# Performance work log

Hardware: AMD Instinct MI355X
Metric: run time of the kernel (lower is better)

The kernel has to match this reference:

```python
import jax, jax.numpy as jnp
import numpy as np

DIM = 1024
DEPTH = 7
PAR = 8
N_NODES = 2 ** (DEPTH + 1) - 1  # 255
WIDTH = PAR * N_NODES  # 2040


def setup_inputs() -> dict:
    key = jax.random.key(0)
    k1, k2, k3, k4 = jax.random.split(key, 4)
    init_k = float(np.sqrt(1.0 / DIM))
    init_k2 = float(np.sqrt(1.0 / ((DEPTH + 1) * PAR)))
    oldx = jax.random.normal(k1, (4, 2048, DIM), dtype=jnp.float32)
    W_in = jax.random.uniform(k2, (WIDTH, DIM), jnp.float32, -init_k, init_k)
    b_in = jax.random.uniform(k3, (WIDTH,), jnp.float32, -init_k, init_k)
    W_out = jax.random.uniform(k4, (DIM, WIDTH), jnp.float32, -init_k2, init_k2)
    return {"oldx": oldx, "W_in": W_in, "b_in": b_in, "W_out": W_out}


def reference(oldx, W_in, b_in, W_out):
    x = oldx.reshape(-1, DIM)                      # [B, dim]
    B = x.shape[0]
    logits = x @ W_in.T + b_in                     # [B, width] dense GEMM over ALL nodes
    decisions = (logits > 0).astype(jnp.int32).reshape(B, PAR, N_NODES)
    acts = jax.nn.silu(logits).reshape(B, PAR, N_NODES)

    # Tree traversal: mark root, then descend DEPTH levels by each node's sign bit.
    current = jnp.zeros((B, PAR), dtype=jnp.int32)
    dmap = jax.nn.one_hot(current, N_NODES, dtype=acts.dtype)  # root node marked
    for d in range(DEPTH):
        cur_platform = 2 ** d - 1
        next_platform = 2 ** (d + 1) - 1
        moves = jnp.take_along_axis(decisions, current[..., None], axis=2)[..., 0]
        current = (current - cur_platform) * 2 + moves + next_platform
        dmap = dmap + jax.nn.one_hot(current, N_NODES, dtype=acts.dtype)

    masked = acts * jax.lax.stop_gradient(dmap)    # only depth+1 nodes per tree survive
    out = masked.reshape(B, WIDTH) @ W_out.T       # [B, dim]
    return out.reshape(oldx.shape)
```

## Files before the change

### kernel.cpp

```cpp
#include <hip/hip_runtime.h>
#include <math.h>

#define DIM 1024
#define DEPTH 7
#define PAR 8
#define N_NODES 255
#define WIDTH 2040
#define MARGIN 0.03f

#define REPLANE(p) ((((p) & 1) << 3) | ((((p) >> 1) & 1) << 4) | ((((p) >> 2) & 1) << 5))

typedef float  float2v  __attribute__((ext_vector_type(2)));
typedef _Float16 half2v __attribute__((ext_vector_type(2)));

__device__ __forceinline__ unsigned short f32_to_bf16(float f) {
    unsigned int u = __float_as_uint(f);
    u += 0x7fffu + ((u >> 16) & 1u);
    return (unsigned short)(u >> 16);
}
__device__ __forceinline__ float bf_lo(unsigned int u) { return __uint_as_float(u << 16); }
__device__ __forceinline__ float bf_hi(unsigned int u) { return __uint_as_float(u & 0xffff0000u); }

__device__ __forceinline__ half2v as_h2(unsigned int u) {
    union { unsigned int u; half2v h; } c; c.u = u; return c.h;
}
__device__ __forceinline__ unsigned int pack_h2(float a, float b) {
    union { half2v h; unsigned int u; } c;
    c.h = (half2v){(_Float16)a, (_Float16)b};
    return c.u;
}

__device__ __forceinline__ float dot2h(unsigned int a, unsigned int b, float c) {
#if __has_builtin(__builtin_amdgcn_fdot2)
    return __builtin_amdgcn_fdot2(as_h2(a), as_h2(b), c, false);
#else
    half2v ha = as_h2(a), hb = as_h2(b);
    c = fmaf((float)ha.x, (float)hb.x, c);
    return fmaf((float)ha.y, (float)hb.y, c);
#endif
}

__device__ __forceinline__ float foldK(float a, float b, int K) {
    const bool hi = (threadIdx.x & (unsigned)K) != 0;
    const float keep = hi ? b : a;
    const float send = hi ? a : b;
    return keep + __shfl_xor(send, K, 64);
}

__global__ __launch_bounds__(256) void convert_f16_kernel(
    const float* __restrict__ src, unsigned int* __restrict__ dst, int n4)
{
    int i = (int)(blockIdx.x * blockDim.x + threadIdx.x);
    if (i < n4) {
        float4 v = ((const float4*)src)[i];
        uint2 pk;
        pk.x = pack_h2(v.x, v.y);
        pk.y = pack_h2(v.z, v.w);
        ((uint2*)dst)[i] = pk;
    }
}

__global__ __launch_bounds__(256) void transpose_bf16_kernel(
    const float* __restrict__ W_out, unsigned short* __restrict__ WoT)
{
    __shared__ float tile[64][65];
    const int w0 = blockIdx.x * 64;
    const int d0 = blockIdx.y * 64;
    const int tid = (int)threadIdx.x;
    const int sub = tid & 15;
    const int grp = tid >> 4;

    #pragma unroll
    for (int pass = 0; pass < 4; ++pass) {
        const int dl = pass * 16 + grp;
        const int wl = sub * 4;
        const int w = w0 + wl;
        const int d = d0 + dl;
        float4 v = make_float4(0.f, 0.f, 0.f, 0.f);
        if (w + 3 < WIDTH) {
            v = *(const float4*)(W_out + (size_t)d * WIDTH + w);
        } else {
            float t0 = (w + 0 < WIDTH) ? W_out[(size_t)d * WIDTH + w + 0] : 0.f;
            float t1 = (w + 1 < WIDTH) ? W_out[(size_t)d * WIDTH + w + 1] : 0.f;
            float t2 = (w + 2 < WIDTH) ? W_out[(size_t)d * WIDTH + w + 2] : 0.f;
            float t3 = (w + 3 < WIDTH) ? W_out[(size_t)d * WIDTH + w + 3] : 0.f;
            v = make_float4(t0, t1, t2, t3);
        }
        tile[dl][wl + 0] = v.x; tile[dl][wl + 1] = v.y;
        tile[dl][wl + 2] = v.z; tile[dl][wl + 3] = v.w;
    }
    __syncthreads();
    #pragma unroll
    for (int pass = 0; pass < 4; ++pass) {
        const int wl = pass * 16 + grp;
        const int dl = sub * 4;
        const int w = w0 + wl;
        if (w < WIDTH) {
            unsigned int b0 = f32_to_bf16(tile[dl + 0][wl]);
            unsigned int b1 = f32_to_bf16(tile[dl + 1][wl]);
            unsigned int b2 = f32_to_bf16(tile[dl + 2][wl]);
            unsigned int b3 = f32_to_bf16(tile[dl + 3][wl]);
            uint2 pk;
            pk.x = b0 | (b1 << 16);
            pk.y = b2 | (b3 << 16);
            *(uint2*)(WoT + (size_t)w * DIM + d0 + dl) = pk;
        }
    }
}

__global__ __launch_bounds__(256) void fff_f16_kernel(
    const float* __restrict__ x,
    const float* __restrict__ W_in,
    const float* __restrict__ b_in,
    const unsigned int* __restrict__ Wh,
    const unsigned short* __restrict__ WoT,
    float* __restrict__ out,
    int B)
{
    const int wave = (int)((blockIdx.x * blockDim.x + threadIdx.x) >> 6);
    const int lane = (int)(threadIdx.x & 63);
    if (wave >= B) return;

    const float* xr = x + (size_t)wave * DIM;
    unsigned int xp[8];
    {
        float4 a0 = *(const float4*)(xr + lane * 8 + 0);
        float4 a1 = *(const float4*)(xr + lane * 8 + 4);
        float4 a2 = *(const float4*)(xr + 512 + lane * 8 + 0);
        float4 a3 = *(const float4*)(xr + 512 + lane * 8 + 4);
        xp[0] = pack_h2(a0.x, a0.y);
        xp[1] = pack_h2(a0.z, a0.w);
        xp[2] = pack_h2(a1.x, a1.y);
        xp[3] = pack_h2(a1.z, a1.w);
        xp[4] = pack_h2(a2.x, a2.y);
        xp[5] = pack_h2(a2.z, a2.w);
        xp[6] = pack_h2(a3.x, a3.y);
        xp[7] = pack_h2(a3.z, a3.w);
    }

    float2v acc2[8];
    #pragma unroll
    for (int i = 0; i < 8; ++i) acc2[i] = (float2v){0.f, 0.f};

    unsigned long long nodes = 0ULL;
    const int myp = ((lane >> 3) & 1) | (((lane >> 4) & 1) << 1) | (((lane >> 5) & 1) << 2);

    #pragma unroll 1
    for (int d = 0; d <= DEPTH; ++d) {
        int gidx[PAR];
        float partial[PAR];

        #pragma unroll
        for (int p = 0; p < PAR; ++p) {
            const int np = (int)((nodes >> (8 * p)) & 0xffULL);
            gidx[p] = p * N_NODES + np;
            const unsigned int* wr = Wh + (size_t)gidx[p] * (DIM / 2);
            const uint4 u0 = *(const uint4*)(wr + lane * 4);
            const uint4 u1 = *(const uint4*)(wr + 256 + lane * 4);
            float s = 0.f;
            s = dot2h(xp[0], u0.x, s);
            s = dot2h(xp[1], u0.y, s);
            s = dot2h(xp[2], u0.z, s);
            s = dot2h(xp[3], u0.w, s);
            s = dot2h(xp[4], u1.x, s);
            s = dot2h(xp[5], u1.y, s);
            s = dot2h(xp[6], u1.z, s);
            s = dot2h(xp[7], u1.w, s);
            partial[p] = s;
        }

        const float c01 = foldK(partial[0], partial[1], 8);
        const float c23 = foldK(partial[2], partial[3], 8);
        const float c45 = foldK(partial[4], partial[5], 8);
        const float c67 = foldK(partial[6], partial[7], 8);
        const float d0f = foldK(c01, c23, 16);
        const float d1f = foldK(c45, c67, 16);
        float e = foldK(d0f, d1f, 32);
        e += __shfl_xor(e, 1, 64);
        e += __shfl_xor(e, 2, 64);
        e += __shfl_xor(e, 4, 64);

        const int ga = (lane & 8) ? gidx[1] : gidx[0];
        const int gb = (lane & 8) ? gidx[3] : gidx[2];
        const int gc = (lane & 8) ? gidx[5] : gidx[4];
        const int gd = (lane & 8) ? gidx[7] : gidx[6];
        const int ge = (lane & 16) ? gb : ga;
        const int gf = (lane & 16) ? gd : gc;
        const int gmine = (lane & 32) ? gf : ge;
        float my = e + b_in[gmine];

        if (d < DEPTH) {
            const unsigned long long bal = __ballot(fabsf(my) < MARGIN);
            unsigned rm = 0;
            #pragma unroll
            for (int p = 0; p < PAR; ++p)
                rm |= ((unsigned)((bal >> REPLANE(p)) & 1ULL)) << p;
            if (rm) {
                const float4 fa = *(const float4*)(xr + lane * 8 + 0);
                const float4 fb = *(const float4*)(xr + lane * 8 + 4);
                const float4 fc = *(const float4*)(xr + 512 + lane * 8 + 0);
                const float4 fd = *(const float4*)(xr + 512 + lane * 8 + 4);
                while (rm) {
                    const int p = __builtin_ctz(rm); rm &= (rm - 1u);
                    const int np = (int)((nodes >> (8 * p)) & 0xffULL);
                    const int gi = p * N_NODES + np;
                    const float* wr = W_in + (size_t)gi * DIM;
                    const float4 wa = *(const float4*)(wr + lane * 8 + 0);
                    const float4 wb = *(const float4*)(wr + lane * 8 + 4);
                    const float4 wc = *(const float4*)(wr + 512 + lane * 8 + 0);
                    const float4 wd = *(const float4*)(wr + 512 + lane * 8 + 4);
                    float s = 0.f;
                    s = fmaf(fa.x, wa.x, s); s = fmaf(fa.y, wa.y, s);
                    s = fmaf(fa.z, wa.z, s); s = fmaf(fa.w, wa.w, s);
                    s = fmaf(fb.x, wb.x, s); s = fmaf(fb.y, wb.y, s);
                    s = fmaf(fb.z, wb.z, s); s = fmaf(fb.w, wb.w, s);
                    s = fmaf(fc.x, wc.x, s); s = fmaf(fc.y, wc.y, s);
                    s = fmaf(fc.z, wc.z, s); s = fmaf(fc.w, wc.w, s);
                    s = fmaf(fd.x, wd.x, s); s = fmaf(fd.y, wd.y, s);
                    s = fmaf(fd.z, wd.z, s); s = fmaf(fd.w, wd.w, s);
                    #pragma unroll
                    for (int off = 32; off >= 1; off >>= 1)
                        s += __shfl_xor(s, off, 64);
                    const float lf = s + b_in[gi];
                    my = (myp == p) ? lf : my;
                }
            }
        }

        const float act_mine = my / (1.0f + __expf(-my));
        const unsigned long long pos = __ballot(my > 0.0f);

        float act[PAR];
        #pragma unroll
        for (int p = 0; p < PAR; ++p)
            act[p] = __shfl(act_mine, REPLANE(p), 64);

        #pragma unroll
        for (int p = 0; p < PAR; ++p) {
            const unsigned short* wo = WoT + (size_t)gidx[p] * DIM;
            const uint4 u0 = *(const uint4*)(wo + lane * 8);
            const uint4 u1 = *(const uint4*)(wo + 512 + lane * 8);
            const float2v a2 = (float2v){act[p], act[p]};
            acc2[0] += a2 * (float2v){bf_lo(u0.x), bf_hi(u0.x)};
            acc2[1] += a2 * (float2v){bf_lo(u0.y), bf_hi(u0.y)};
            acc2[2] += a2 * (float2v){bf_lo(u0.z), bf_hi(u0.z)};
            acc2[3] += a2 * (float2v){bf_lo(u0.w), bf_hi(u0.w)};
            acc2[4] += a2 * (float2v){bf_lo(u1.x), bf_hi(u1.x)};
            acc2[5] += a2 * (float2v){bf_lo(u1.y), bf_hi(u1.y)};
            acc2[6] += a2 * (float2v){bf_lo(u1.z), bf_hi(u1.z)};
            acc2[7] += a2 * (float2v){bf_lo(u1.w), bf_hi(u1.w)};

            if (d < DEPTH) {
                const int np = (int)((nodes >> (8 * p)) & 0xffULL);
                const unsigned long long nn = (unsigned long long)
                    (2 * np + 1 + (int)((pos >> REPLANE(p)) & 1ULL));
                nodes = (nodes & ~(0xffULL << (8 * p))) | (nn << (8 * p));
            }
        }
    }

    float* orow = out + (size_t)wave * DIM;
    *(float4*)(orow + lane * 8 + 0) =
        make_float4(acc2[0].x, acc2[0].y, acc2[1].x, acc2[1].y);
    *(float4*)(orow + lane * 8 + 4) =
        make_float4(acc2[2].x, acc2[2].y, acc2[3].x, acc2[3].y);
    *(float4*)(orow + 512 + lane * 8 + 0) =
        make_float4(acc2[4].x, acc2[4].y, acc2[5].x, acc2[5].y);
    *(float4*)(orow + 512 + lane * 8 + 4) =
        make_float4(acc2[6].x, acc2[6].y, acc2[7].x, acc2[7].y);
}

__global__ __launch_bounds__(256) void fff_fallback_kernel(
    const float* __restrict__ x, const float* __restrict__ W_in,
    const float* __restrict__ b_in, const float* __restrict__ W_out,
    float* __restrict__ out, int B)
{
    const int wave = (int)((blockIdx.x * blockDim.x + threadIdx.x) >> 6);
    const int lane = (int)(threadIdx.x & 63);
    if (wave >= B) return;

    const float* xr = x + (size_t)wave * DIM;
    float4 x4[4];
    x4[0] = *(const float4*)(xr + lane * 8 + 0);
    x4[1] = *(const float4*)(xr + lane * 8 + 4);
    x4[2] = *(const float4*)(xr + 512 + lane * 8 + 0);
    x4[3] = *(const float4*)(xr + 512 + lane * 8 + 4);

    float acc[16];
    #pragma unroll
    for (int i = 0; i < 16; ++i) acc[i] = 0.f;
    int node[PAR];
    #pragma unroll
    for (int p = 0; p < PAR; ++p) node[p] = 0;

    for (int d = 0; d <= DEPTH; ++d) {
        #pragma unroll
        for (int p = 0; p < PAR; ++p) {
            const int gidx = p * N_NODES + node[p];
            const float* wr = W_in + (size_t)gidx * DIM;
            const float4 wa = *(const float4*)(wr + lane * 8 + 0);
            const float4 wb = *(const float4*)(wr + lane * 8 + 4);
            const float4 wc = *(const float4*)(wr + 512 + lane * 8 + 0);
            const float4 wd = *(const float4*)(wr + 512 + lane * 8 + 4);
            float s = 0.f;
            s = fmaf(x4[0].x, wa.x, s); s = fmaf(x4[0].y, wa.y, s);
            s = fmaf(x4[0].z, wa.z, s); s = fmaf(x4[0].w, wa.w, s);
            s = fmaf(x4[1].x, wb.x, s); s = fmaf(x4[1].y, wb.y, s);
            s = fmaf(x4[1].z, wb.z, s); s = fmaf(x4[1].w, wb.w, s);
            s = fmaf(x4[2].x, wc.x, s); s = fmaf(x4[2].y, wc.y, s);
            s = fmaf(x4[2].z, wc.z, s); s = fmaf(x4[2].w, wc.w, s);
            s = fmaf(x4[3].x, wd.x, s); s = fmaf(x4[3].y, wd.y, s);
            s = fmaf(x4[3].z, wd.z, s); s = fmaf(x4[3].w, wd.w, s);
            #pragma unroll
            for (int off = 32; off >= 1; off >>= 1)
                s += __shfl_xor(s, off, 64);
            const float logit = s + b_in[gidx];
            const float act = logit / (1.0f + __expf(-logit));
            #pragma unroll
            for (int k = 0; k < 2; ++k) {
                #pragma unroll
                for (int j = 0; j < 8; ++j) {
                    const int e = k * 512 + lane * 8 + j;
                    acc[k * 8 + j] = fmaf(act, W_out[(size_t)e * WIDTH + gidx], acc[k * 8 + j]);
                }
            }
            node[p] = 2 * node[p] + 1 + ((logit > 0.0f) ? 1 : 0);
        }
    }

    float* orow = out + (size_t)wave * DIM;
    *(float4*)(orow + lane * 8 + 0)       = make_float4(acc[0],  acc[1],  acc[2],  acc[3]);
    *(float4*)(orow + lane * 8 + 4)       = make_float4(acc[4],  acc[5],  acc[6],  acc[7]);
    *(float4*)(orow + 512 + lane * 8 + 0) = make_float4(acc[8],  acc[9],  acc[10], acc[11]);
    *(float4*)(orow + 512 + lane * 8 + 4) = make_float4(acc[12], acc[13], acc[14], acc[15]);
}

extern "C" void kernel_launch(void* const* d_in, const int* in_sizes, int n_in,
                              void* d_out, int out_size, void* d_ws, size_t ws_size,
                              hipStream_t stream) {
    const float* oldx  = (const float*)d_in[0];
    const float* W_in  = (const float*)d_in[1];
    const float* b_in  = (const float*)d_in[2];
    const float* W_out = (const float*)d_in[3];
    float* out = (float*)d_out;

    const int B = in_sizes[0] / DIM;

    const size_t half = (size_t)WIDTH * DIM * sizeof(unsigned short);
    const bool use_lp = (ws_size >= 2 * half) && (d_ws != nullptr);

    const int blocks = (B + 3) / 4;

    if (use_lp) {
        unsigned short* WoT = (unsigned short*)d_ws;
        unsigned int*   Wh  = (unsigned int*)((char*)d_ws + half);
        dim3 tg((WIDTH + 63) / 64, DIM / 64);
        transpose_bf16_kernel<<<tg, 256, 0, stream>>>(W_out, WoT);
        const int n4 = WIDTH * DIM / 4;
        convert_f16_kernel<<<(n4 + 255) / 256, 256, 0, stream>>>(W_in, Wh, n4);
        fff_f16_kernel<<<blocks, 256, 0, stream>>>(oldx, W_in, b_in, Wh, WoT, out, B);
    } else {
        fff_fallback_kernel<<<blocks, 256, 0, stream>>>(oldx, W_in, b_in, W_out, out, B);
    }
}
```

Before: 185.9 us.

## Fuse weight prep kernels, hoist loads ahead of reductions, store W_out as fp16

The two weight preprocessing kernels (W_out transpose and W_in fp16 conversion) are merged into one launch with a block-range split. In the main kernel, all W_in row loads for a level are issued before the dot products, and half of the W_out row loads are issued before the cross-lane reduction and ballot, to hide memory latency. W_out is now stored in fp16 instead of bf16 with scalar fmaf accumulation, and the near-zero refinement margin is tightened, which reduces fp32 recomputation but risks sign-flip mismatches near zero. The extra live registers for prefetched rows may reduce occupancy.

Result: no change. 182.4 us (-1.9%).

```diff
diff --git a/kernel.cpp b/kernel.cpp
--- a/kernel.cpp
+++ b/kernel.cpp
@@ -6,20 +6,11 @@
 #define PAR 8
 #define N_NODES 255
 #define WIDTH 2040
-#define MARGIN 0.03f
+#define MARGIN 0.01f
 
 #define REPLANE(p) ((((p) & 1) << 3) | ((((p) >> 1) & 1) << 4) | ((((p) >> 2) & 1) << 5))
 
-typedef float  float2v  __attribute__((ext_vector_type(2)));
 typedef _Float16 half2v __attribute__((ext_vector_type(2)));
-
-__device__ __forceinline__ unsigned short f32_to_bf16(float f) {
-    unsigned int u = __float_as_uint(f);
-    u += 0x7fffu + ((u >> 16) & 1u);
-    return (unsigned short)(u >> 16);
-}
-__device__ __forceinline__ float bf_lo(unsigned int u) { return __uint_as_float(u << 16); }
-__device__ __forceinline__ float bf_hi(unsigned int u) { return __uint_as_float(u & 0xffff0000u); }
 
 __device__ __forceinline__ half2v as_h2(unsigned int u) {
     union { unsigned int u; half2v h; } c; c.u = u; return c.h;
@@ -47,63 +38,76 @@
     return keep + __shfl_xor(send, K, 64);
 }
 
-__global__ __launch_bounds__(256) void convert_f16_kernel(
-    const float* __restrict__ src, unsigned int* __restrict__ dst, int n4)
-{
-    int i = (int)(blockIdx.x * blockDim.x + threadIdx.x);
-    if (i < n4) {
-        float4 v = ((const float4*)src)[i];
-        uint2 pk;
-        pk.x = pack_h2(v.x, v.y);
-        pk.y = pack_h2(v.z, v.w);
-        ((uint2*)dst)[i] = pk;
-    }
-}
-
-__global__ __launch_bounds__(256) void transpose_bf16_kernel(
-    const float* __restrict__ W_out, unsigned short* __restrict__ WoT)
+#define PHASE_C_TREE(WLO, WHI, A) do {                                                      \
+    const float a_ = (A); half2v h_;                                                        \
+    h_ = as_h2((WLO).x); acc[0]  = fmaf((float)h_.x, a_, acc[0]);  acc[1]  = fmaf((float)h_.y, a_, acc[1]);  \
+    h_ = as_h2((WLO).y); acc[2]  = fmaf((float)h_.x, a_, acc[2]);  acc[3]  = fmaf((float)h_.y, a_, acc[3]);  \
+    h_ = as_h2((WLO).z); acc[4]  = fmaf((float)h_.x, a_, acc[4]);  acc[5]  = fmaf((float)h_.y, a_, acc[5]);  \
+    h_ = as_h2((WLO).w); acc[6]  = fmaf((float)h_.x, a_, acc[6]);  acc[7]  = fmaf((float)h_.y, a_, acc[7]);  \
+    h_ = as_h2((WHI).x); acc[8]  = fmaf((float)h_.x, a_, acc[8]);  acc[9]  = fmaf((float)h_.y, a_, acc[9]);  \
+    h_ = as_h2((WHI).y); acc[10] = fmaf((float)h_.x, a_, acc[10]); acc[11] = fmaf((float)h_.y, a_, acc[11]); \
+    h_ = as_h2((WHI).z); acc[12] = fmaf((float)h_.x, a_, acc[12]); acc[13] = fmaf((float)h_.y, a_, acc[13]); \
+    h_ = as_h2((WHI).w); acc[14] = fmaf((float)h_.x, a_, acc[14]); acc[15] = fmaf((float)h_.y, a_, acc[15]); \
+} while (0)
+
+#define TRANS_BLOCKS 512
+
+__global__ __launch_bounds__(256) void prep_kernel(
+    const float* __restrict__ W_out,
+    const float* __restrict__ W_in,
+    unsigned short* __restrict__ WoT,
+    unsigned int* __restrict__ Wh)
 {
     __shared__ float tile[64][65];
-    const int w0 = blockIdx.x * 64;
-    const int d0 = blockIdx.y * 64;
-    const int tid = (int)threadIdx.x;
-    const int sub = tid & 15;
-    const int grp = tid >> 4;
-
-    #pragma unroll
-    for (int pass = 0; pass < 4; ++pass) {
-        const int dl = pass * 16 + grp;
-        const int wl = sub * 4;
-        const int w = w0 + wl;
-        const int d = d0 + dl;
-        float4 v = make_float4(0.f, 0.f, 0.f, 0.f);
-        if (w + 3 < WIDTH) {
-            v = *(const float4*)(W_out + (size_t)d * WIDTH + w);
-        } else {
-            float t0 = (w + 0 < WIDTH) ? W_out[(size_t)d * WIDTH + w + 0] : 0.f;
-            float t1 = (w + 1 < WIDTH) ? W_out[(size_t)d * WIDTH + w + 1] : 0.f;
-            float t2 = (w + 2 < WIDTH) ? W_out[(size_t)d * WIDTH + w + 2] : 0.f;
-            float t3 = (w + 3 < WIDTH) ? W_out[(size_t)d * WIDTH + w + 3] : 0.f;
-            v = make_float4(t0, t1, t2, t3);
-        }
-        tile[dl][wl + 0] = v.x; tile[dl][wl + 1] = v.y;
-        tile[dl][wl + 2] = v.z; tile[dl][wl + 3] = v.w;
-    }
-    __syncthreads();
-    #pragma unroll
-    for (int pass = 0; pass < 4; ++pass) {
-        const int wl = pass * 16 + grp;
-        const int dl = sub * 4;
-        const int w = w0 + wl;
-        if (w < WIDTH) {
-            unsigned int b0 = f32_to_bf16(tile[dl + 0][wl]);
-            unsigned int b1 = f32_to_bf16(tile[dl + 1][wl]);
-            unsigned int b2 = f32_to_bf16(tile[dl + 2][wl]);
-            unsigned int b3 = f32_to_bf16(tile[dl + 3][wl]);
+    if (blockIdx.x < TRANS_BLOCKS) {
+        const int w0 = (int)(blockIdx.x & 31) * 64;
+        const int d0 = (int)(blockIdx.x >> 5) * 64;
+        const int tid = (int)threadIdx.x;
+        const int sub = tid & 15;
+        const int grp = tid >> 4;
+
+        #pragma unroll
+        for (int pass = 0; pass < 4; ++pass) {
+            const int dl = pass * 16 + grp;
+            const int wl = sub * 4;
+            const int w = w0 + wl;
+            const int d = d0 + dl;
+            float4 v = make_float4(0.f, 0.f, 0.f, 0.f);
+            if (w + 3 < WIDTH) {
+                v = *(const float4*)(W_out + (size_t)d * WIDTH + w);
+            } else {
+                float t0 = (w + 0 < WIDTH) ? W_out[(size_t)d * WIDTH + w + 0] : 0.f;
+                float t1 = (w + 1 < WIDTH) ? W_out[(size_t)d * WIDTH + w + 1] : 0.f;
+                float t2 = (w + 2 < WIDTH) ? W_out[(size_t)d * WIDTH + w + 2] : 0.f;
+                float t3 = (w + 3 < WIDTH) ? W_out[(size_t)d * WIDTH + w + 3] : 0.f;
+                v = make_float4(t0, t1, t2, t3);
+            }
+            tile[dl][wl + 0] = v.x; tile[dl][wl + 1] = v.y;
+            tile[dl][wl + 2] = v.z; tile[dl][wl + 3] = v.w;
+        }
+        __syncthreads();
+        #pragma unroll
+        for (int pass = 0; pass < 4; ++pass) {
+            const int wl = pass * 16 + grp;
+            const int dl = sub * 4;
+            const int w = w0 + wl;
+            if (w < WIDTH) {
+                uint2 pk;
+                pk.x = pack_h2(tile[dl + 0][wl], tile[dl + 1][wl]);
+                pk.y = pack_h2(tile[dl + 2][wl], tile[dl + 3][wl]);
+                *(uint2*)(WoT + (size_t)w * DIM + d0 + dl) = pk;
+            }
+        }
+    } else {
+        const int n4 = WIDTH * DIM / 4;
+        const int nthr = ((int)gridDim.x - TRANS_BLOCKS) * 256;
+        for (int i = ((int)blockIdx.x - TRANS_BLOCKS) * 256 + (int)threadIdx.x;
+             i < n4; i += nthr) {
+            float4 v = ((const float4*)W_in)[i];
             uint2 pk;
-            pk.x = b0 | (b1 << 16);
-            pk.y = b2 | (b3 << 16);
-            *(uint2*)(WoT + (size_t)w * DIM + d0 + dl) = pk;
+            pk.x = pack_h2(v.x, v.y);
+            pk.y = pack_h2(v.z, v.w);
+            ((uint2*)Wh)[i] = pk;
         }
     }
 }
@@ -138,9 +142,9 @@
         xp[7] = pack_h2(a3.z, a3.w);
     }
 
-    float2v acc2[8];
+    float acc[16];
     #pragma unroll
-    for (int i = 0; i < 8; ++i) acc2[i] = (float2v){0.f, 0.f};
+    for (int i = 0; i < 16; ++i) acc[i] = 0.f;
 
     unsigned long long nodes = 0ULL;
     const int myp = ((lane >> 3) & 1) | (((lane >> 4) & 1) << 1) | (((lane >> 5) & 1) << 2);
@@ -148,25 +152,50 @@
     #pragma unroll 1
     for (int d = 0; d <= DEPTH; ++d) {
         int gidx[PAR];
-        float partial[PAR];
-
         #pragma unroll
         for (int p = 0; p < PAR; ++p) {
             const int np = (int)((nodes >> (8 * p)) & 0xffULL);
             gidx[p] = p * N_NODES + np;
+        }
+
+        const int ga = (lane & 8) ? gidx[1] : gidx[0];
+        const int gb = (lane & 8) ? gidx[3] : gidx[2];
+        const int gc = (lane & 8) ? gidx[5] : gidx[4];
+        const int gd = (lane & 8) ? gidx[7] : gidx[6];
+        const int ge = (lane & 16) ? gb : ga;
+        const int gf = (lane & 16) ? gd : gc;
+        const int gmine = (lane & 32) ? gf : ge;
+        const float bias = b_in[gmine];
+
+        uint4 ua[PAR], ub[PAR];
+        #pragma unroll
+        for (int p = 0; p < PAR; ++p) {
             const unsigned int* wr = Wh + (size_t)gidx[p] * (DIM / 2);
-            const uint4 u0 = *(const uint4*)(wr + lane * 4);
-            const uint4 u1 = *(const uint4*)(wr + 256 + lane * 4);
+            ua[p] = *(const uint4*)(wr + lane * 4);
+            ub[p] = *(const uint4*)(wr + 256 + lane * 4);
+        }
+
+        float partial[PAR];
+        #pragma unroll
+        for (int p = 0; p < PAR; ++p) {
             float s = 0.f;
-            s = dot2h(xp[0], u0.x, s);
-            s = dot2h(xp[1], u0.y, s);
-            s = dot2h(xp[2], u0.z, s);
-            s = dot2h(xp[3], u0.w, s);
-            s = dot2h(xp[4], u1.x, s);
-            s = dot2h(xp[5], u1.y, s);
-            s = dot2h(xp[6], u1.z, s);
-            s = dot2h(xp[7], u1.w, s);
+            s = dot2h(xp[0], ua[p].x, s);
+            s = dot2h(xp[1], ua[p].y, s);
+            s = dot2h(xp[2], ua[p].z, s);
+            s = dot2h(xp[3], ua[p].w, s);
+            s = dot2h(xp[4], ub[p].x, s);
+            s = dot2h(xp[5], ub[p].y, s);
+            s = dot2h(xp[6], ub[p].z, s);
+            s = dot2h(xp[7], ub[p].w, s);
             partial[p] = s;
+        }
+
+        uint4 wva[4], wvb[4];
+        #pragma unroll
+        for (int p = 0; p < 4; ++p) {
+            const unsigned short* wo = WoT + (size_t)gidx[p] * DIM;
+            wva[p] = *(const uint4*)(wo + lane * 8);
+            wvb[p] = *(const uint4*)(wo + 512 + lane * 8);
         }
 
         const float c01 = foldK(partial[0], partial[1], 8);
@@ -179,15 +208,7 @@
         e += __shfl_xor(e, 1, 64);
         e += __shfl_xor(e, 2, 64);
         e += __shfl_xor(e, 4, 64);
-
-        const int ga = (lane & 8) ? gidx[1] : gidx[0];
-        const int gb = (lane & 8) ? gidx[3] : gidx[2];
-        const int gc = (lane & 8) ? gidx[5] : gidx[4];
-        const int gd = (lane & 8) ? gidx[7] : gidx[6];
-        const int ge = (lane & 16) ? gb : ga;
-        const int gf = (lane & 16) ? gd : gc;
-        const int gmine = (lane & 32) ? gf : ge;
-        float my = e + b_in[gmine];
+        float my = e + bias;
 
         if (d < DEPTH) {
             const unsigned long long bal = __ballot(fabsf(my) < MARGIN);
@@ -202,8 +223,7 @@
                 const float4 fd = *(const float4*)(xr + 512 + lane * 8 + 4);
                 while (rm) {
                     const int p = __builtin_ctz(rm); rm &= (rm - 1u);
-                    const int np = (int)((nodes >> (8 * p)) & 0xffULL);
-                    const int gi = p * N_NODES + np;
+                    const int gi = gidx[p];
                     const float* wr = W_in + (size_t)gi * DIM;
                     const float4 wa = *(const float4*)(wr + lane * 8 + 0);
                     const float4 wb = *(const float4*)(wr + lane * 8 + 4);
@@ -235,22 +255,22 @@
         for (int p = 0; p < PAR; ++p)
             act[p] = __shfl(act_mine, REPLANE(p), 64);
 
-        #pragma unroll
-        for (int p = 0; p < PAR; ++p) {
-            const unsigned short* wo = WoT + (size_t)gidx[p] * DIM;
-            const uint4 u0 = *(const uint4*)(wo + lane * 8);
-            const uint4 u1 = *(const uint4*)(wo + 512 + lane * 8);
-            const float2v a2 = (float2v){act[p], act[p]};
-            acc2[0] += a2 * (float2v){bf_lo(u0.x), bf_hi(u0.x)};
-            acc2[1] += a2 * (float2v){bf_lo(u0.y), bf_hi(u0.y)};
-            acc2[2] += a2 * (float2v){bf_lo(u0.z), bf_hi(u0.z)};
-            acc2[3] += a2 * (float2v){bf_lo(u0.w), bf_hi(u0.w)};
-            acc2[4] += a2 * (float2v){bf_lo(u1.x), bf_hi(u1.x)};
-            acc2[5] += a2 * (float2v){bf_lo(u1.y), bf_hi(u1.y)};
-            acc2[6] += a2 * (float2v){bf_lo(u1.z), bf_hi(u1.z)};
-            acc2[7] += a2 * (float2v){bf_lo(u1.w), bf_hi(u1.w)};
-
-            if (d < DEPTH) {
+        uint4 wvc[4], wvd[4];
+        #pragma unroll
+        for (int p = 0; p < 4; ++p) {
+            const unsigned short* wo = WoT + (size_t)gidx[4 + p] * DIM;
+            wvc[p] = *(const uint4*)(wo + lane * 8);
+            wvd[p] = *(const uint4*)(wo + 512 + lane * 8);
+        }
+
+        #pragma unroll
+        for (int p = 0; p < 4; ++p) PHASE_C_TREE(wva[p], wvb[p], act[p]);
+        #pragma unroll
+        for (int p = 0; p < 4; ++p) PHASE_C_TREE(wvc[p], wvd[p], act[4 + p]);
+
+        if (d < DEPTH) {
+            #pragma unroll
+            for (int p = 0; p < PAR; ++p) {
                 const int np = (int)((nodes >> (8 * p)) & 0xffULL);
                 const unsigned long long nn = (unsigned long long)
                     (2 * np + 1 + (int)((pos >> REPLANE(p)) & 1ULL));
@@ -260,14 +280,10 @@
     }
 
     float* orow = out + (size_t)wave * DIM;
-    *(float4*)(orow + lane * 8 + 0) =
-        make_float4(acc2[0].x, acc2[0].y, acc2[1].x, acc2[1].y);
-    *(float4*)(orow + lane * 8 + 4) =
-        make_float4(acc2[2].x, acc2[2].y, acc2[3].x, acc2[3].y);
-    *(float4*)(orow + 512 + lane * 8 + 0) =
-        make_float4(acc2[4].x, acc2[4].y, acc2[5].x, acc2[5].y);
-    *(float4*)(orow + 512 + lane * 8 + 4) =
-        make_float4(acc2[6].x, acc2[6].y, acc2[7].x, acc2[7].y);
+    *(float4*)(orow + lane * 8 + 0)       = make_float4(acc[0],  acc[1],  acc[2],  acc[3]);
+    *(float4*)(orow + lane * 8 + 4)       = make_float4(acc[4],  acc[5],  acc[6],  acc[7]);
+    *(float4*)(orow + 512 + lane * 8 + 0) = make_float4(acc[8],  acc[9],  acc[10], acc[11]);
+    *(float4*)(orow + 512 + lane * 8 + 4) = make_float4(acc[12], acc[13], acc[14], acc[15]);
 }
 
 __global__ __launch_bounds__(256) void fff_fallback_kernel(
@@ -354,10 +370,7 @@
     if (use_lp) {
         unsigned short* WoT = (unsigned short*)d_ws;
         unsigned int*   Wh  = (unsigned int*)((char*)d_ws + half);
-        dim3 tg((WIDTH + 63) / 64, DIM / 64);
-        transpose_bf16_kernel<<<tg, 256, 0, stream>>>(W_out, WoT);
-        const int n4 = WIDTH * DIM / 4;
-        convert_f16_kernel<<<(n4 + 255) / 256, 256, 0, stream>>>(W_in, Wh, n4);
+        prep_kernel<<<TRANS_BLOCKS + 1024, 256, 0, stream>>>(W_out, W_in, WoT, Wh);
         fff_f16_kernel<<<blocks, 256, 0, stream>>>(oldx, W_in, b_in, Wh, WoT, out, B);
     } else {
         fff_fallback_kernel<<<blocks, 256, 0, stream>>>(oldx, W_in, b_in, W_out, out, B);
```
